# Optimization experiments

Measured on AMD Instinct MI355X. Metric: run time of the kernel, lower is better.

The kernel has to match this reference:

```python
import jax, jax.numpy as jnp
import numpy as np

MAX_SEQ_LEN = 4096
N_QUBITS = 11
N_LAYERS = 2
DIM = 2 ** N_QUBITS


def setup_inputs() -> dict:
    key = jax.random.key(0)
    k_theta, = jax.random.split(key, 1)
    # matches nn.Parameter(torch.randn(max_seq_len, n_layers, 3*n_qubits) * 0.1)
    theta = jax.random.normal(k_theta, (MAX_SEQ_LEN, N_LAYERS, 3 * N_QUBITS), dtype=jnp.float32) * 0.1
    positions = jnp.arange(MAX_SEQ_LEN, dtype=jnp.int32)
    return {"theta": theta, "positions": positions}


def _gate_matrices(theta_sel):
    """theta_sel: (B, L, 3Q) -> combined single-qubit unitaries U = Rz @ Ry @ Rx, (B, L, Q, 2, 2) complex64."""
    B = theta_sel.shape[0]
    ang = theta_sel.reshape(B, N_LAYERS, N_QUBITS, 3) * 0.5  # half angles
    a, b, g = ang[..., 0], ang[..., 1], ang[..., 2]  # rx, ry, rz
    ca, sa = jnp.cos(a), jnp.sin(a)
    cb, sb = jnp.cos(b), jnp.sin(b)
    zero = jnp.zeros_like(a) + 0j
    # RX(t) = [[cos t/2, -i sin t/2], [-i sin t/2, cos t/2]]
    Rx = jnp.stack([jnp.stack([ca + 0j, -1j * sa], -1),
                    jnp.stack([-1j * sa, ca + 0j], -1)], -2)
    # RY(t) = [[cos, -sin], [sin, cos]]
    Ry = jnp.stack([jnp.stack([cb + 0j, -sb + 0j], -1),
                    jnp.stack([sb + 0j, cb + 0j], -1)], -2)
    # RZ(t) = diag(e^{-it/2}, e^{+it/2})
    Rz = jnp.stack([jnp.stack([jnp.exp(-1j * g), zero], -1),
                    jnp.stack([zero, jnp.exp(1j * g)], -1)], -2)
    return jnp.einsum('...ij,...jk,...kl->...il', Rz, Ry, Rx).astype(jnp.complex64)


def _simulate(theta_sel):
    """Batched little-endian statevector simulation of the PQC. Returns (B, 2^Q) float32 (real part)."""
    B = theta_sel.shape[0]
    U = _gate_matrices(theta_sel)  # (B, L, Q, 2, 2)
    state = jnp.zeros((B, DIM), jnp.complex64).at[:, 0].set(1.0)  # |0...0>
    for l in range(N_LAYERS):
        # single-qubit RX.RY.RZ block (fused per qubit)
        for q in range(N_QUBITS):
            # qubit q has stride 2^q in little-endian index
            st = state.reshape(B, 2 ** (N_QUBITS - 1 - q), 2, 2 ** q)
            state = jnp.einsum('bij,bhjl->bhil', U[:, l, q], st).reshape(B, DIM)
        # CX ladder: cx(q, q+1) -> control bit q, target bit q+1
        for q in range(N_QUBITS - 1):
            st = state.reshape(B, 2 ** (N_QUBITS - 2 - q), 2, 2, 2 ** q)  # (B, rest, target, control, low)
            c0 = st[:, :, :, 0, :]
            c1 = st[:, :, ::-1, 1, :]  # flip target when control = 1
            state = jnp.stack([c0, c1], axis=3).reshape(B, DIM)
    return state.real.astype(jnp.float32)


def reference(theta, positions):
    return _simulate(theta[positions])
```

## Files before the change

### kernel.cpp

```cpp
#include <hip/hip_runtime.h>
#include <math.h>

#define N_QUBITS 11
#define DIM 2048


struct cT { float r0, i0, r1, i1; };

static __device__ __forceinline__
cT step(const float* Krow, const cT& T)
{
    const float4 A = *(const float4*)(Krow);
    const float4 B = *(const float4*)(Krow + 4);
    cT o;
    o.r0 = A.x * T.r0 - A.y * T.i0 + A.z * T.r1 - A.w * T.i1;
    o.i0 = A.x * T.i0 + A.y * T.r0 + A.z * T.i1 + A.w * T.r1;
    o.r1 = B.x * T.r0 - B.y * T.i0 + B.z * T.r1 - B.w * T.i1;
    o.i1 = B.x * T.i0 + B.y * T.r0 + B.z * T.i1 + B.w * T.r1;
    return o;
}

static __device__ __forceinline__
float redot(const float4& m, const cT& T)
{
    return m.x * T.r0 - m.y * T.i0 + m.z * T.r1 - m.w * T.i1;
}

__global__ __launch_bounds__(128)
void pqc_sim_kernel(const float* __restrict__ theta,
                    const int* __restrict__ positions,
                    float* __restrict__ out)
{
    __shared__ float C1[N_QUBITS][4];
    __shared__ float G2[N_QUBITS][8];
    __shared__ float K[N_QUBITS][2][8];
    __shared__ float UM[2][2][4];

    const int t   = threadIdx.x;
    const int b   = blockIdx.x;
    const int pos = positions[b];

    if (t < 22) {
        const int l = t / N_QUBITS;
        const int q = t % N_QUBITS;
        const float* th = theta + (((size_t)pos * 2 + l) * (3 * N_QUBITS)) + 3 * q;
        const float a  = th[0] * 0.5f;
        const float bb = th[1] * 0.5f;
        const float g  = th[2] * 0.5f;
        float sa, ca, sb, cb, sg, cg;
        sincosf(a,  &sa, &ca);
        sincosf(bb, &sb, &cb);
        sincosf(g,  &sg, &cg);
        const float m00r =  cb * ca, m00i =  sb * sa;
        const float m01r = -sb * ca, m01i = -cb * sa;
        const float m10r =  sb * ca, m10i = -cb * sa;
        const float m11r =  cb * ca, m11i = -sb * sa;
        const float u00r = m00r * cg + m00i * sg, u00i = m00i * cg - m00r * sg;
        const float u01r = m01r * cg + m01i * sg, u01i = m01i * cg - m01r * sg;
        const float u10r = m10r * cg - m10i * sg, u10i = m10i * cg + m10r * sg;
        const float u11r = m11r * cg - m11i * sg, u11i = m11i * cg + m11r * sg;
        if (l) {
            G2[q][0] = u00r; G2[q][1] = u00i; G2[q][2] = u01r; G2[q][3] = u01i;
            G2[q][4] = u10r; G2[q][5] = u10i; G2[q][6] = u11r; G2[q][7] = u11i;
        } else {
            C1[q][0] = u00r; C1[q][1] = u00i;
            C1[q][2] = u10r; C1[q][3] = u10i;
        }
    }
    __syncthreads();

    if (t < 44) {
        const int q = t >> 1, bb = t & 1;
        const float v0r = G2[q][bb * 4 + 0], v0i = G2[q][bb * 4 + 1];
        const float v1r = G2[q][bb * 4 + 2], v1i = G2[q][bb * 4 + 3];
        const float c0r = C1[q][0], c0i = C1[q][1];
        const float c1r = C1[q][2], c1i = C1[q][3];
        K[q][bb][0] = v0r * c0r - v0i * c0i;
        K[q][bb][1] = v0r * c0i + v0i * c0r;
        K[q][bb][2] = v1r * c1r - v1i * c1i;
        K[q][bb][3] = v1r * c1i + v1i * c1r;
        K[q][bb][4] = v0r * c1r - v0i * c1i;
        K[q][bb][5] = v0r * c1i + v0i * c1r;
        K[q][bb][6] = v1r * c0r - v1i * c0i;
        K[q][bb][7] = v1r * c0i + v1i * c0r;
    }
    __syncthreads();

    if (t < 4) {
        const int n0 = t >> 1, bb = t & 1;
        const float u0r = K[0][n0][0], u0i = K[0][n0][1];
        const float u1r = K[0][n0][2], u1i = K[0][n0][3];
        const float d0r = K[1][bb][0], d0i = K[1][bb][1];
        const float d1r = K[1][bb][2], d1i = K[1][bb][3];
        const float e0r = K[1][bb][4], e0i = K[1][bb][5];
        const float e1r = K[1][bb][6], e1i = K[1][bb][7];
        UM[n0][bb][0] = u0r * d0r - u0i * d0i + u1r * e0r - u1i * e0i;
        UM[n0][bb][1] = u0r * d0i + u0i * d0r + u1r * e0i + u1i * e0r;
        UM[n0][bb][2] = u0r * d1r - u0i * d1i + u1r * e1r - u1i * e1i;
        UM[n0][bb][3] = u0r * d1i + u0i * d1r + u1r * e1i + u1i * e1r;
    }
    __syncthreads();

    const int w = t >> 6, L = t & 63;

    cT T;
    {
        const float* Kr = &K[10][w ^ (L >> 5)][0];
        const float4 A = *(const float4*)(Kr);
        const float4 B = *(const float4*)(Kr + 4);
        T.r0 = A.x + A.z;  T.i0 = A.y + A.w;
        T.r1 = B.x + B.z;  T.i1 = B.y + B.w;
    }
    const int z = L ^ (L >> 1);
    #pragma unroll
    for (int k = 4; k >= 0; --k) {
        T = step(&K[5 + k][(z >> k) & 1][0], T);
    }

    const float4 um00 = *(const float4*)&UM[0][0][0];
    const float4 um01 = *(const float4*)&UM[0][1][0];
    const float4 um10 = *(const float4*)&UM[1][0][0];
    const float4 um11 = *(const float4*)&UM[1][1][0];
    const int L0 = L & 1;
    float* orow = out + (size_t)b * DIM + w * 1024 + L * 16;

    #pragma unroll
    for (int n3 = 0; n3 < 2; ++n3) {
        const cT T4 = step(&K[4][L0 ^ n3][0], T);
        #pragma unroll
        for (int n2 = 0; n2 < 2; ++n2) {
            const cT T3  = step(&K[3][n3 ^ n2][0], T4);
            const cT T2a = step(&K[2][n2][0],     T3);
            const cT T2b = step(&K[2][n2 ^ 1][0], T3);
            float4 o;
            o.x = redot(um00, T2a);
            o.y = redot(um11, T2a);
            o.z = redot(um01, T2b);
            o.w = redot(um10, T2b);
            *(float4*)(orow + 4 * n2 + 8 * n3) = o;
        }
    }
}

extern "C" void kernel_launch(void* const* d_in, const int* in_sizes, int n_in,
                              void* d_out, int out_size, void* d_ws, size_t ws_size,
                              hipStream_t stream)
{
    const float* theta     = (const float*)d_in[0];
    const int*   positions = (const int*)d_in[1];
    float*       out       = (float*)d_out;
    const int B = in_sizes[1];

    pqc_sim_kernel<<<B, 128, 0, stream>>>(theta, positions, out);
}
```

Baseline: 76.33 us.

## Precompute shared high-qubit partial products and fold qubit-2 into output matrices

Builds a 64-entry shared table of the partial product over qubits 5-10, computed once per block by 64 threads. Each thread then does a single lookup instead of repeating five complex steps. Qubit 2 is also folded into eight combined output vectors (UM3), which removes the two per-output K2 steps. The setup phase is redistributed so both wavefronts participate. The cost is more shared memory and more setup work before the sync, in exchange for less per-thread arithmetic in the output loop.

```diff
diff --git a/kernel.cpp b/kernel.cpp
--- a/kernel.cpp
+++ b/kernel.cpp
@@ -21,6 +21,17 @@
 }
 
 static __device__ __forceinline__
+cT stepv(const float4 A, const float4 B, const cT& T)
+{
+    cT o;
+    o.r0 = A.x * T.r0 - A.y * T.i0 + A.z * T.r1 - A.w * T.i1;
+    o.i0 = A.x * T.i0 + A.y * T.r0 + A.z * T.i1 + A.w * T.r1;
+    o.r1 = B.x * T.r0 - B.y * T.i0 + B.z * T.r1 - B.w * T.i1;
+    o.i1 = B.x * T.i0 + B.y * T.r0 + B.z * T.i1 + B.w * T.r1;
+    return o;
+}
+
+static __device__ __forceinline__
 float redot(const float4& m, const cT& T)
 {
     return m.x * T.r0 - m.y * T.i0 + m.z * T.r1 - m.w * T.i1;
@@ -31,18 +42,19 @@
                     const int* __restrict__ positions,
                     float* __restrict__ out)
 {
-    __shared__ float C1[N_QUBITS][4];
-    __shared__ float G2[N_QUBITS][8];
-    __shared__ float K[N_QUBITS][2][8];
-    __shared__ float UM[2][2][4];
+    __shared__ float  C1[N_QUBITS][4];
+    __shared__ float  G2[N_QUBITS][8];
+    __shared__ float  K[N_QUBITS][2][8];
+    __shared__ float4 W6[64];
+    __shared__ float4 UM3[8];
 
     const int t   = threadIdx.x;
     const int b   = blockIdx.x;
     const int pos = positions[b];
 
-    if (t < 22) {
-        const int l = t / N_QUBITS;
-        const int q = t % N_QUBITS;
+    if ((t & 63) < N_QUBITS) {
+        const int l = t >> 6;
+        const int q = t & 63;
         const float* th = theta + (((size_t)pos * 2 + l) * (3 * N_QUBITS)) + 3 * q;
         const float a  = th[0] * 0.5f;
         const float bb = th[1] * 0.5f;
@@ -69,8 +81,9 @@
     }
     __syncthreads();
 
-    if (t < 44) {
-        const int q = t >> 1, bb = t & 1;
+    if ((t & 63) < N_QUBITS) {
+        const int q  = t & 63;
+        const int bb = t >> 6;
         const float v0r = G2[q][bb * 4 + 0], v0i = G2[q][bb * 4 + 1];
         const float v1r = G2[q][bb * 4 + 2], v1i = G2[q][bb * 4 + 3];
         const float c0r = C1[q][0], c0i = C1[q][1];
@@ -86,58 +99,94 @@
     }
     __syncthreads();
 
-    if (t < 4) {
-        const int n0 = t >> 1, bb = t & 1;
+    if ((t & 63) < 32) {
+        const int e = (t & 63) | ((t >> 6) << 5);
+        const float* Kr = &K[10][e >> 5][0];
+        const float4 A = *(const float4*)(Kr);
+        const float4 B = *(const float4*)(Kr + 4);
+        cT T;
+        T.r0 = A.x + A.z;  T.i0 = A.y + A.w;
+        T.r1 = B.x + B.z;  T.i1 = B.y + B.w;
+        T = step(&K[9][(e >> 4) & 1][0], T);
+        T = step(&K[8][(e >> 3) & 1][0], T);
+        T = step(&K[7][(e >> 2) & 1][0], T);
+        T = step(&K[6][(e >> 1) & 1][0], T);
+        T = step(&K[5][e & 1][0], T);
+        W6[e] = make_float4(T.r0, T.i0, T.r1, T.i1);
+    } else if (t >= 32 && t < 40) {
+        const int e  = t - 32;
+        const int n0 = e >> 2, n1 = (e >> 1) & 1, b2 = e & 1;
+        const int b1 = n1 ^ n0;
         const float u0r = K[0][n0][0], u0i = K[0][n0][1];
         const float u1r = K[0][n0][2], u1i = K[0][n0][3];
-        const float d0r = K[1][bb][0], d0i = K[1][bb][1];
-        const float d1r = K[1][bb][2], d1i = K[1][bb][3];
-        const float e0r = K[1][bb][4], e0i = K[1][bb][5];
-        const float e1r = K[1][bb][6], e1i = K[1][bb][7];
-        UM[n0][bb][0] = u0r * d0r - u0i * d0i + u1r * e0r - u1i * e0i;
-        UM[n0][bb][1] = u0r * d0i + u0i * d0r + u1r * e0i + u1i * e0r;
-        UM[n0][bb][2] = u0r * d1r - u0i * d1i + u1r * e1r - u1i * e1i;
-        UM[n0][bb][3] = u0r * d1i + u0i * d1r + u1r * e1i + u1i * e1r;
+        const float d0r = K[1][b1][0], d0i = K[1][b1][1];
+        const float d1r = K[1][b1][2], d1i = K[1][b1][3];
+        const float e0r = K[1][b1][4], e0i = K[1][b1][5];
+        const float e1r = K[1][b1][6], e1i = K[1][b1][7];
+        const float r0r = u0r * d0r - u0i * d0i + u1r * e0r - u1i * e0i;
+        const float r0i = u0r * d0i + u0i * d0r + u1r * e0i + u1i * e0r;
+        const float r1r = u0r * d1r - u0i * d1i + u1r * e1r - u1i * e1i;
+        const float r1i = u0r * d1i + u0i * d1r + u1r * e1i + u1i * e1r;
+        const float f0r = K[2][b2][0], f0i = K[2][b2][1];
+        const float f1r = K[2][b2][2], f1i = K[2][b2][3];
+        const float g0r = K[2][b2][4], g0i = K[2][b2][5];
+        const float g1r = K[2][b2][6], g1i = K[2][b2][7];
+        const float s0r = r0r * f0r - r0i * f0i + r1r * g0r - r1i * g0i;
+        const float s0i = r0r * f0i + r0i * f0r + r1r * g0i + r1i * g0r;
+        const float s1r = r0r * f1r - r0i * f1i + r1r * g1r - r1i * g1i;
+        const float s1i = r0r * f1i + r0i * f1r + r1r * g1i + r1i * g1r;
+        UM3[e] = make_float4(s0r, s0i, s1r, s1i);
     }
     __syncthreads();
 
     const int w = t >> 6, L = t & 63;
-
-    cT T;
+    const int z = L ^ (L >> 1);
+    const int widx = ((w ^ (L >> 5)) << 5) | (z & 31);
+    const float4 Tv = W6[widx];
+    cT T; T.r0 = Tv.x; T.i0 = Tv.y; T.r1 = Tv.z; T.i1 = Tv.w;
+
+    const float4 m0 = UM3[0], m1 = UM3[1], m2 = UM3[2], m3 = UM3[3];
+    const float4 m4 = UM3[4], m5 = UM3[5], m6 = UM3[6], m7 = UM3[7];
+    const float4 k3A0 = *(const float4*)&K[3][0][0], k3B0 = *(const float4*)&K[3][0][4];
+    const float4 k3A1 = *(const float4*)&K[3][1][0], k3B1 = *(const float4*)&K[3][1][4];
+
+    const int L0 = L & 1;
+    const float* k4a = &K[4][L0][0];
+    const float* k4b = &K[4][L0 ^ 1][0];
+    float* orow = out + (size_t)b * DIM + w * 1024 + L * 16;
+
     {
-        const float* Kr = &K[10][w ^ (L >> 5)][0];
-        const float4 A = *(const float4*)(Kr);
-        const float4 B = *(const float4*)(Kr + 4);
-        T.r0 = A.x + A.z;  T.i0 = A.y + A.w;
-        T.r1 = B.x + B.z;  T.i1 = B.y + B.w;
-    }
-    const int z = L ^ (L >> 1);
-    #pragma unroll
-    for (int k = 4; k >= 0; --k) {
-        T = step(&K[5 + k][(z >> k) & 1][0], T);
-    }
-
-    const float4 um00 = *(const float4*)&UM[0][0][0];
-    const float4 um01 = *(const float4*)&UM[0][1][0];
-    const float4 um10 = *(const float4*)&UM[1][0][0];
-    const float4 um11 = *(const float4*)&UM[1][1][0];
-    const int L0 = L & 1;
-    float* orow = out + (size_t)b * DIM + w * 1024 + L * 16;
-
-    #pragma unroll
-    for (int n3 = 0; n3 < 2; ++n3) {
-        const cT T4 = step(&K[4][L0 ^ n3][0], T);
-        #pragma unroll
-        for (int n2 = 0; n2 < 2; ++n2) {
-            const cT T3  = step(&K[3][n3 ^ n2][0], T4);
-            const cT T2a = step(&K[2][n2][0],     T3);
-            const cT T2b = step(&K[2][n2 ^ 1][0], T3);
-            float4 o;
-            o.x = redot(um00, T2a);
-            o.y = redot(um11, T2a);
-            o.z = redot(um01, T2b);
-            o.w = redot(um10, T2b);
-            *(float4*)(orow + 4 * n2 + 8 * n3) = o;
+        const cT T4 = step(k4a, T);
+        {
+            const cT T3 = stepv(k3A0, k3B0, T4);
+            float4 o;
+            o.x = redot(m0, T3);  o.y = redot(m4, T3);
+            o.z = redot(m3, T3);  o.w = redot(m7, T3);
+            *(float4*)(orow + 0) = o;
+        }
+        {
+            const cT T3 = stepv(k3A1, k3B1, T4);
+            float4 o;
+            o.x = redot(m1, T3);  o.y = redot(m5, T3);
+            o.z = redot(m2, T3);  o.w = redot(m6, T3);
+            *(float4*)(orow + 4) = o;
+        }
+    }
+    {
+        const cT T4 = step(k4b, T);
+        {
+            const cT T3 = stepv(k3A1, k3B1, T4);
+            float4 o;
+            o.x = redot(m0, T3);  o.y = redot(m4, T3);
+            o.z = redot(m3, T3);  o.w = redot(m7, T3);
+            *(float4*)(orow + 8) = o;
+        }
+        {
+            const cT T3 = stepv(k3A0, k3B0, T4);
+            float4 o;
+            o.x = redot(m1, T3);  o.y = redot(m5, T3);
+            o.z = redot(m2, T3);  o.w = redot(m6, T3);
+            *(float4*)(orow + 12) = o;
         }
     }
 }
```

Result: no change. 76.92 us (+0.8%).
